# Kernel optimization log

Measured on AMD Instinct MI355X. Metric: run time of the kernel, lower is better.

## Reference

```python
import jax, jax.numpy as jnp
import numpy as np

N = 50000          # nodes
E = 800000         # edges (before self loops)
H = 4              # attention heads
C = 64             # per-head channels
D_IN = 256
NEG_ATT = 0.2      # GATConv attention LeakyReLU slope
NEG_ACT = 0.01     # nn.LeakyReLU default slope
EPS = 1e-5
MLP_DIMS = [64, 32, 16, 2]


def _gat_layer(x, src, dst, W, a_src, a_dst, b, concat):
    """PyG GATConv: gather -> segment-softmax over dst -> scatter-add."""
    n = x.shape[0]
    h = (x @ W).reshape(n, H, C)                       # [N,H,C]
    s = (h * a_src).sum(-1)                            # [N,H]
    d = (h * a_dst).sum(-1)                            # [N,H]
    e = jax.nn.leaky_relu(s[src] + d[dst], NEG_ATT)    # [E',H]
    m = jax.ops.segment_max(e, dst, num_segments=n)    # per-dst max (self loops -> no empty segs)
    w = jnp.exp(e - m[dst])
    den = jax.ops.segment_sum(w, dst, num_segments=n)
    alpha = w / den[dst]                               # [E',H]
    out = jax.ops.segment_sum(alpha[:, :, None] * h[src], dst, num_segments=n)  # [N,H,C]
    out = out.reshape(n, H * C) if concat else out.mean(axis=1)
    return out + b


def _graph_norm(x, w, b, a):
    mu = x.mean(axis=0, keepdims=True)
    y = x - a * mu
    var = (y * y).mean(axis=0, keepdims=True)
    return w * y * jax.lax.rsqrt(var + EPS) + b


def setup_inputs() -> dict:
    key = jax.random.key(0)
    ks = jax.random.split(key, 40)
    d = {
        'x': jax.random.normal(ks[0], (N, D_IN), dtype=jnp.float32),
        'edge_index': jax.random.randint(ks[1], (2, E), 0, N, dtype=jnp.int64),
    }
    dims_in = [D_IN, H * C, H * C]
    norm_dims = [H * C, H * C, C]
    k = 2
    for i in range(3):
        fan = dims_in[i]
        d[f'W{i}'] = jax.random.normal(ks[k], (fan, H * C), dtype=jnp.float32) / np.sqrt(fan); k += 1
        d[f'as{i}'] = jax.random.normal(ks[k], (H, C), dtype=jnp.float32) / np.sqrt(C); k += 1
        d[f'ad{i}'] = jax.random.normal(ks[k], (H, C), dtype=jnp.float32) / np.sqrt(C); k += 1
        d[f'b{i}'] = jnp.zeros((norm_dims[i],), dtype=jnp.float32)
        d[f'gw{i}'] = jnp.ones((norm_dims[i],), dtype=jnp.float32)
        d[f'gb{i}'] = jnp.zeros((norm_dims[i],), dtype=jnp.float32)
        d[f'ga{i}'] = jnp.ones((norm_dims[i],), dtype=jnp.float32)
    for j in range(3):
        fi, fo = MLP_DIMS[j], MLP_DIMS[j + 1]
        d[f'mW{j}'] = jax.random.normal(ks[k], (fi, fo), dtype=jnp.float32) / np.sqrt(fi); k += 1
        d[f'mb{j}'] = jnp.zeros((fo,), dtype=jnp.float32)
    return d


def reference(x, edge_index,
              W0, as0, ad0, b0, gw0, gb0, ga0,
              W1, as1, ad1, b1, gw1, gb1, ga1,
              W2, as2, ad2, b2, gw2, gb2, ga2,
              mW0, mb0, mW1, mb1, mW2, mb2):
    n = x.shape[0]
    loop = jnp.arange(n, dtype=edge_index.dtype)
    src = jnp.concatenate([edge_index[0], loop])   # add self loops (PyG default)
    dst = jnp.concatenate([edge_index[1], loop])

    h = _gat_layer(x, src, dst, W0, as0, ad0, b0, concat=True)
    h = jax.nn.leaky_relu(_graph_norm(h, gw0, gb0, ga0), NEG_ACT)
    h = _gat_layer(h, src, dst, W1, as1, ad1, b1, concat=True)
    h = jax.nn.leaky_relu(_graph_norm(h, gw1, gb1, ga1), NEG_ACT)
    h = _gat_layer(h, src, dst, W2, as2, ad2, b2, concat=False)
    h = jax.nn.leaky_relu(_graph_norm(h, gw2, gb2, ga2), NEG_ACT)

    h = jax.nn.relu(h @ mW0 + mb0)
    h = jax.nn.relu(h @ mW1 + mb1)
    return h @ mW2 + mb2
```

## Files before the change

kernel.cpp:

```cpp
#include <hip/hip_runtime.h>

#define NN 50000
#define EE 800000
#define ET 850000
#define HH 4
#define CC 64
#define FDIM 256

#define SCAN_BLK 512
#define SCAN_NB ((NN + SCAN_BLK - 1) / SCAN_BLK)

typedef unsigned short ushort;
typedef __bf16 bf16x8 __attribute__((ext_vector_type(8)));
typedef float floatx4 __attribute__((ext_vector_type(4)));
typedef ushort ushort8v __attribute__((ext_vector_type(8)));
struct ushort4s { ushort x, y, z, w; };

__device__ __forceinline__ ushort f2bf(float f) {
  union { float f; unsigned u; } v; v.f = f;
  unsigned r = v.u + 0x7fffu + ((v.u >> 16) & 1u);
  return (ushort)(r >> 16);
}
__device__ __forceinline__ float bf2f(ushort u) {
  return __uint_as_float(((unsigned)u) << 16);
}

__device__ __forceinline__ int get_edge(const void* p, int is64, long long idx) {
  if (is64) return (int)((const long long*)p)[idx];
  return ((const int*)p)[idx];
}

__global__ void detect_kernel(const unsigned int* p, int* flag) {
  __shared__ unsigned red[256];
  int t = threadIdx.x;
  unsigned o = 0;
  for (int i = 0; i < 4; i++) o |= p[(t * 4 + i) * 2 + 1];
  red[t] = o;
  __syncthreads();
  for (int s = 128; s > 0; s >>= 1) {
    if (t < s) red[t] |= red[t + s];
    __syncthreads();
  }
  if (t == 0) *flag = (red[0] == 0) ? 1 : 0;
}

__global__ void degree_kernel(const void* eidx, const int* flag, int* deg) {
  int k = blockIdx.x * blockDim.x + threadIdx.x;
  if (k >= ET) return;
  int is64 = *flag;
  int dst = (k < EE) ? get_edge(eidx, is64, (long long)EE + k) : (k - EE);
  atomicAdd(&deg[dst], 1);
}

__global__ __launch_bounds__(SCAN_BLK) void scan1_kernel(const int* __restrict__ deg,
                                                         int* __restrict__ rowptr,
                                                         int* __restrict__ bsum) {
  __shared__ int sm[SCAN_BLK];
  int t = threadIdx.x;
  int i = blockIdx.x * SCAN_BLK + t;
  int v = (i < NN) ? deg[i] : 0;
  sm[t] = v;
  __syncthreads();
#pragma unroll
  for (int o = 1; o < SCAN_BLK; o <<= 1) {
    int u = (t >= o) ? sm[t - o] : 0;
    __syncthreads();
    sm[t] += u;
    __syncthreads();
  }
  if (i < NN) rowptr[i] = sm[t] - v;
  if (t == SCAN_BLK - 1) bsum[blockIdx.x] = sm[t];
}

__global__ __launch_bounds__(128) void scan2_kernel(const int* __restrict__ bsum,
                                                    int* __restrict__ boff,
                                                    int* __restrict__ rowptr) {
  __shared__ int sm[128];
  int t = threadIdx.x;
  int v = (t < SCAN_NB) ? bsum[t] : 0;
  sm[t] = v;
  __syncthreads();
#pragma unroll
  for (int o = 1; o < 128; o <<= 1) {
    int u = (t >= o) ? sm[t - o] : 0;
    __syncthreads();
    sm[t] += u;
    __syncthreads();
  }
  if (t < SCAN_NB) boff[t] = sm[t] - v;
  if (t == 0) rowptr[NN] = ET;
}

__global__ __launch_bounds__(SCAN_BLK) void scan3_kernel(int* __restrict__ rowptr,
                                                         int* __restrict__ cursor,
                                                         const int* __restrict__ boff) {
  int i = blockIdx.x * SCAN_BLK + threadIdx.x;
  if (i >= NN) return;
  int v = rowptr[i] + boff[blockIdx.x];
  rowptr[i] = v;
  cursor[i] = v;
}

__global__ void fill_kernel(const void* eidx, const int* flag, int* cursor, int* csr_src) {
  int k = blockIdx.x * blockDim.x + threadIdx.x;
  if (k >= ET) return;
  int is64 = *flag;
  int src, dst;
  if (k < EE) {
    src = get_edge(eidx, is64, k);
    dst = get_edge(eidx, is64, (long long)EE + k);
  } else {
    src = dst = k - EE;
  }
  int pos = atomicAdd(&cursor[dst], 1);
  csr_src[pos] = src;
}

__global__ void conv_x_kernel(const float* __restrict__ x, ushort* __restrict__ xb) {
  int i = blockIdx.x * 256 + threadIdx.x;
  float4 v = ((const float4*)x)[i];
  ushort4s o;
  o.x = f2bf(v.x); o.y = f2bf(v.y); o.z = f2bf(v.z); o.w = f2bf(v.w);
  ((ushort4s*)xb)[i] = o;
}

__global__ void conv_w_kernel(const float* __restrict__ W, ushort* __restrict__ Wt) {
  int idx = blockIdx.x * 256 + threadIdx.x;
  int k = idx >> 8, n = idx & 255;
  Wt[n * 256 + k] = f2bf(W[idx]);
}

__global__ __launch_bounds__(256) void gemm_bf16(const ushort* __restrict__ A,
                                                 const ushort* __restrict__ Bt,
                                                 ushort* __restrict__ C) {
  __shared__ ushort As[8 * 512];
  __shared__ ushort Bs[8 * 512];
  int tid = threadIdx.x, w = tid >> 6, l = tid & 63;
  int brow0 = blockIdx.x * 128, bcol0 = blockIdx.y * 128;
  int lm = l & 15, lk = (l >> 4) * 8;
  int s0 = 2 * w, s1 = 2 * w + 1;
  int ar0 = min(brow0 + s0 * 16 + lm, NN - 1);
  int ar1 = min(brow0 + s1 * 16 + lm, NN - 1);
  const ushort* ag0 = A + (size_t)ar0 * 256 + lk;
  const ushort* ag1 = A + (size_t)ar1 * 256 + lk;
  const ushort* bg0 = Bt + (size_t)(bcol0 + s0 * 16 + lm) * 256 + lk;
  const ushort* bg1 = Bt + (size_t)(bcol0 + s1 * 16 + lm) * 256 + lk;

  floatx4 acc[4][4];
#pragma unroll
  for (int i = 0; i < 4; i++)
#pragma unroll
    for (int j = 0; j < 4; j++) acc[i][j] = floatx4{0.f, 0.f, 0.f, 0.f};

  int wm = (w >> 1) * 4, wn = (w & 1) * 4;

  for (int k0 = 0; k0 < 256; k0 += 32) {
    ushort8v a0 = *(const ushort8v*)(ag0 + k0);
    ushort8v a1 = *(const ushort8v*)(ag1 + k0);
    ushort8v b0 = *(const ushort8v*)(bg0 + k0);
    ushort8v b1 = *(const ushort8v*)(bg1 + k0);
    *(ushort8v*)&As[s0 * 512 + l * 8] = a0;
    *(ushort8v*)&As[s1 * 512 + l * 8] = a1;
    *(ushort8v*)&Bs[s0 * 512 + l * 8] = b0;
    *(ushort8v*)&Bs[s1 * 512 + l * 8] = b1;
    __syncthreads();
    bf16x8 af[4], bfr[4];
#pragma unroll
    for (int i = 0; i < 4; i++) af[i] = *(const bf16x8*)&As[(wm + i) * 512 + l * 8];
#pragma unroll
    for (int j = 0; j < 4; j++) bfr[j] = *(const bf16x8*)&Bs[(wn + j) * 512 + l * 8];
#pragma unroll
    for (int i = 0; i < 4; i++)
#pragma unroll
      for (int j = 0; j < 4; j++)
        acc[i][j] = __builtin_amdgcn_mfma_f32_16x16x32_bf16(af[i], bfr[j], acc[i][j], 0, 0, 0);
    __syncthreads();
  }

  int quad = l >> 4;
#pragma unroll
  for (int i = 0; i < 4; i++) {
    int r0 = brow0 + (wm + i) * 16 + quad * 4;
#pragma unroll
    for (int j = 0; j < 4; j++) {
      int col = bcol0 + (wn + j) * 16 + lm;
#pragma unroll
      for (int r = 0; r < 4; r++) {
        int row = r0 + r;
        if (row < NN) C[(size_t)row * 256 + col] = f2bf(acc[i][j][r]);
      }
    }
  }
}

__global__ __launch_bounds__(256) void sd_kernel(const ushort* __restrict__ h,
                                                 const float* __restrict__ as_,
                                                 const float* __restrict__ ad_,
                                                 float* __restrict__ s, float* __restrict__ d) {
  int w = threadIdx.x >> 6;
  int l = threadIdx.x & 63;
  int n = blockIdx.x * 4 + w;
  ushort4s hv = *(const ushort4s*)(h + (size_t)n * FDIM + l * 4);
  float4 av = ((const float4*)as_)[l];
  float4 dv = ((const float4*)ad_)[l];
  float f0 = bf2f(hv.x), f1 = bf2f(hv.y), f2 = bf2f(hv.z), f3 = bf2f(hv.w);
  float ps = f0 * av.x + f1 * av.y + f2 * av.z + f3 * av.w;
  float pd = f0 * dv.x + f1 * dv.y + f2 * dv.z + f3 * dv.w;
#pragma unroll
  for (int o = 1; o < 16; o <<= 1) {
    ps += __shfl_xor(ps, o);
    pd += __shfl_xor(pd, o);
  }
  if ((l & 15) == 0) {
    s[n * HH + (l >> 4)] = ps;
    d[n * HH + (l >> 4)] = pd;
  }
}

template <bool CONCAT>
__global__ __launch_bounds__(256) void agg_kernel(const ushort* __restrict__ hb,
                                                  const float* __restrict__ s_arr,
                                                  const float* __restrict__ d_arr,
                                                  const int* __restrict__ rowptr,
                                                  const int* __restrict__ csr_src,
                                                  const float* __restrict__ bias,
                                                  void* __restrict__ outp) {
  int w = __builtin_amdgcn_readfirstlane(threadIdx.x >> 6);
  int l = threadIdx.x & 63;
  int head = l >> 4;
  int n = blockIdx.x * 4 + w;
  int beg = rowptr[n], end = rowptr[n + 1];
  float dh = d_arr[n * HH + head];
  float a0 = 0.f, a1 = 0.f, a2 = 0.f, a3 = 0.f, den = 0.f;

  int i = beg;
  for (; i + 4 <= end; i += 4) {
    int s0 = csr_src[i], s1 = csr_src[i + 1], s2 = csr_src[i + 2], s3 = csr_src[i + 3];
    float e0 = s_arr[s0 * HH + head] + dh;
    float e1 = s_arr[s1 * HH + head] + dh;
    float e2 = s_arr[s2 * HH + head] + dh;
    float e3 = s_arr[s3 * HH + head] + dh;
    ushort4s h0 = *(const ushort4s*)(hb + (unsigned)(s0 * FDIM + l * 4));
    ushort4s h1 = *(const ushort4s*)(hb + (unsigned)(s1 * FDIM + l * 4));
    ushort4s h2 = *(const ushort4s*)(hb + (unsigned)(s2 * FDIM + l * 4));
    ushort4s h3 = *(const ushort4s*)(hb + (unsigned)(s3 * FDIM + l * 4));
    e0 = (e0 > 0.f) ? e0 : 0.2f * e0;  float w0 = __expf(e0);
    e1 = (e1 > 0.f) ? e1 : 0.2f * e1;  float w1 = __expf(e1);
    e2 = (e2 > 0.f) ? e2 : 0.2f * e2;  float w2 = __expf(e2);
    e3 = (e3 > 0.f) ? e3 : 0.2f * e3;  float w3 = __expf(e3);
    den += (w0 + w1) + (w2 + w3);
    a0 = fmaf(w0, bf2f(h0.x), a0); a1 = fmaf(w0, bf2f(h0.y), a1);
    a2 = fmaf(w0, bf2f(h0.z), a2); a3 = fmaf(w0, bf2f(h0.w), a3);
    a0 = fmaf(w1, bf2f(h1.x), a0); a1 = fmaf(w1, bf2f(h1.y), a1);
    a2 = fmaf(w1, bf2f(h1.z), a2); a3 = fmaf(w1, bf2f(h1.w), a3);
    a0 = fmaf(w2, bf2f(h2.x), a0); a1 = fmaf(w2, bf2f(h2.y), a1);
    a2 = fmaf(w2, bf2f(h2.z), a2); a3 = fmaf(w2, bf2f(h2.w), a3);
    a0 = fmaf(w3, bf2f(h3.x), a0); a1 = fmaf(w3, bf2f(h3.y), a1);
    a2 = fmaf(w3, bf2f(h3.z), a2); a3 = fmaf(w3, bf2f(h3.w), a3);
  }
  for (; i < end; i++) {
    int s0 = csr_src[i];
    float e0 = s_arr[s0 * HH + head] + dh;
    ushort4s h0 = *(const ushort4s*)(hb + (unsigned)(s0 * FDIM + l * 4));
    e0 = (e0 > 0.f) ? e0 : 0.2f * e0;
    float w0 = __expf(e0);
    den += w0;
    a0 = fmaf(w0, bf2f(h0.x), a0); a1 = fmaf(w0, bf2f(h0.y), a1);
    a2 = fmaf(w0, bf2f(h0.z), a2); a3 = fmaf(w0, bf2f(h0.w), a3);
  }
  float inv = 1.0f / den;
  float r0 = a0 * inv, r1 = a1 * inv, r2 = a2 * inv, r3 = a3 * inv;

  if (CONCAT) {
    float4 bv = ((const float4*)bias)[l];
    ushort4s o;
    o.x = f2bf(r0 + bv.x); o.y = f2bf(r1 + bv.y);
    o.z = f2bf(r2 + bv.z); o.w = f2bf(r3 + bv.w);
    ((ushort4s*)outp)[(unsigned)(n * 64 + l)] = o;
  } else {
    r0 += __shfl_xor(r0, 16); r1 += __shfl_xor(r1, 16);
    r2 += __shfl_xor(r2, 16); r3 += __shfl_xor(r3, 16);
    r0 += __shfl_xor(r0, 32); r1 += __shfl_xor(r1, 32);
    r2 += __shfl_xor(r2, 32); r3 += __shfl_xor(r3, 32);
    if (l < 16) {
      float4 bv = ((const float4*)bias)[l];
      float4 o;
      o.x = 0.25f * r0 + bv.x; o.y = 0.25f * r1 + bv.y;
      o.z = 0.25f * r2 + bv.z; o.w = 0.25f * r3 + bv.w;
      ((float4*)outp)[(unsigned)(n * 16 + l)] = o;
    }
  }
}

__global__ __launch_bounds__(256) void norm_reduce_bf(const ushort* __restrict__ xin,
                                                      float* colsum, float* colsumsq) {
  int f = threadIdx.x;
  int r0 = blockIdx.x * 128;
  int r1 = min(NN, r0 + 128);
  float s1 = 0.f, s2 = 0.f;
  for (int r = r0; r < r1; r++) {
    float v = bf2f(xin[(size_t)r * FDIM + f]);
    s1 += v; s2 += v * v;
  }
  atomicAdd(&colsum[f], s1);
  atomicAdd(&colsumsq[f], s2);
}

__global__ __launch_bounds__(256) void norm_reduce_f32(const float* __restrict__ xin,
                                                       float* colsum, float* colsumsq) {
  int f = threadIdx.x & (CC - 1);
  int rl = threadIdx.x / CC;
  int r0 = blockIdx.x * 128;
  int r1 = min(NN, r0 + 128);
  float s1 = 0.f, s2 = 0.f;
  for (int r = r0 + rl; r < r1; r += 4) {
    float v = xin[(size_t)r * CC + f];
    s1 += v; s2 += v * v;
  }
  atomicAdd(&colsum[f], s1);
  atomicAdd(&colsumsq[f], s2);
}

__global__ __launch_bounds__(256) void norm_apply_bf(const ushort* __restrict__ in,
                                                     ushort* __restrict__ outb,
                                                     const float* __restrict__ colsum,
                                                     const float* __restrict__ colsumsq,
                                                     const float* __restrict__ ga,
                                                     const float* __restrict__ gw,
                                                     const float* __restrict__ gb) {
  __shared__ float sc[FDIM], sh[FDIM];
  int t = threadIdx.x;
  {
    const float invn = 1.0f / (float)NN;
    float mu = colsum[t] * invn;
    float ex2 = colsumsq[t] * invn;
    float a = ga[t];
    float var = fmaxf(ex2 - (2.f * a - a * a) * mu * mu, 0.f);
    float s = gw[t] * rsqrtf(var + 1e-5f);
    sc[t] = s; sh[t] = gb[t] - s * a * mu;
  }
  __syncthreads();
  const int total = NN * FDIM / 4;
  for (int i = blockIdx.x * 256 + t; i < total; i += gridDim.x * 256) {
    int f0 = (i * 4) & (FDIM - 1);
    ushort4s v = ((const ushort4s*)in)[i];
    float y0 = sc[f0 + 0] * bf2f(v.x) + sh[f0 + 0];
    float y1 = sc[f0 + 1] * bf2f(v.y) + sh[f0 + 1];
    float y2 = sc[f0 + 2] * bf2f(v.z) + sh[f0 + 2];
    float y3 = sc[f0 + 3] * bf2f(v.w) + sh[f0 + 3];
    ushort4s o;
    o.x = f2bf((y0 > 0.f) ? y0 : 0.01f * y0);
    o.y = f2bf((y1 > 0.f) ? y1 : 0.01f * y1);
    o.z = f2bf((y2 > 0.f) ? y2 : 0.01f * y2);
    o.w = f2bf((y3 > 0.f) ? y3 : 0.01f * y3);
    ((ushort4s*)outb)[i] = o;
  }
}

__global__ __launch_bounds__(256) void norm_apply_f32(float* __restrict__ xio,
                                                      const float* __restrict__ colsum,
                                                      const float* __restrict__ colsumsq,
                                                      const float* __restrict__ ga,
                                                      const float* __restrict__ gw,
                                                      const float* __restrict__ gb) {
  __shared__ float sc[CC], sh[CC];
  int t = threadIdx.x;
  if (t < CC) {
    const float invn = 1.0f / (float)NN;
    float mu = colsum[t] * invn;
    float ex2 = colsumsq[t] * invn;
    float a = ga[t];
    float var = fmaxf(ex2 - (2.f * a - a * a) * mu * mu, 0.f);
    float s = gw[t] * rsqrtf(var + 1e-5f);
    sc[t] = s; sh[t] = gb[t] - s * a * mu;
  }
  __syncthreads();
  const int total = NN * CC;
  for (int i = blockIdx.x * 256 + t; i < total; i += gridDim.x * 256) {
    int f = i & (CC - 1);
    float y = sc[f] * xio[i] + sh[f];
    xio[i] = (y > 0.f) ? y : 0.01f * y;
  }
}

__global__ __launch_bounds__(256) void mlp_kernel(const float* __restrict__ xin,
                                                  const float* mW0, const float* mb0,
                                                  const float* mW1, const float* mb1,
                                                  const float* mW2, const float* mb2,
                                                  float* __restrict__ out) {
  __shared__ float W0s[64 * 32];
  __shared__ float W1s[32 * 16];
  __shared__ float W2s[16 * 2];
  __shared__ float b0s[32], b1s[16], b2s[2];
  int t = threadIdx.x;
  for (int i = t; i < 2048; i += 256) W0s[i] = mW0[i];
  for (int i = t; i < 512; i += 256) W1s[i] = mW1[i];
  if (t < 32) { W2s[t] = mW2[t]; b0s[t] = mb0[t]; }
  if (t < 16) b1s[t] = mb1[t];
  if (t < 2) b2s[t] = mb2[t];
  __syncthreads();
  int node = blockIdx.x * 256 + t;
  if (node >= NN) return;
  float in[64];
  const float* xr = xin + (size_t)node * 64;
#pragma unroll
  for (int k = 0; k < 64; k++) in[k] = xr[k];
  float h1[32];
#pragma unroll
  for (int j = 0; j < 32; j++) h1[j] = b0s[j];
#pragma unroll
  for (int k = 0; k < 64; k++) {
    float v = in[k];
#pragma unroll
    for (int j = 0; j < 32; j++) h1[j] += v * W0s[k * 32 + j];
  }
#pragma unroll
  for (int j = 0; j < 32; j++) h1[j] = fmaxf(h1[j], 0.f);
  float h2[16];
#pragma unroll
  for (int j = 0; j < 16; j++) h2[j] = b1s[j];
#pragma unroll
  for (int k = 0; k < 32; k++) {
    float v = h1[k];
#pragma unroll
    for (int j = 0; j < 16; j++) h2[j] += v * W1s[k * 16 + j];
  }
#pragma unroll
  for (int j = 0; j < 16; j++) h2[j] = fmaxf(h2[j], 0.f);
  float o0 = b2s[0], o1 = b2s[1];
#pragma unroll
  for (int k = 0; k < 16; k++) {
    o0 += h2[k] * W2s[k * 2 + 0];
    o1 += h2[k] * W2s[k * 2 + 1];
  }
  out[(size_t)node * 2 + 0] = o0;
  out[(size_t)node * 2 + 1] = o1;
}

extern "C" void kernel_launch(void* const* d_in, const int* in_sizes, int n_in,
                              void* d_out, int out_size, void* d_ws, size_t ws_size,
                              hipStream_t stream) {
  const float* x = (const float*)d_in[0];
  const void* ei = d_in[1];
  const float* W[3]   = {(const float*)d_in[2],  (const float*)d_in[9],  (const float*)d_in[16]};
  const float* as_[3] = {(const float*)d_in[3],  (const float*)d_in[10], (const float*)d_in[17]};
  const float* ad_[3] = {(const float*)d_in[4],  (const float*)d_in[11], (const float*)d_in[18]};
  const float* b_[3]  = {(const float*)d_in[5],  (const float*)d_in[12], (const float*)d_in[19]};
  const float* gw[3]  = {(const float*)d_in[6],  (const float*)d_in[13], (const float*)d_in[20]};
  const float* gb[3]  = {(const float*)d_in[7],  (const float*)d_in[14], (const float*)d_in[21]};
  const float* ga[3]  = {(const float*)d_in[8],  (const float*)d_in[15], (const float*)d_in[22]};
  const float* mW0 = (const float*)d_in[23];
  const float* mb0 = (const float*)d_in[24];
  const float* mW1 = (const float*)d_in[25];
  const float* mb1 = (const float*)d_in[26];
  const float* mW2 = (const float*)d_in[27];
  const float* mb2 = (const float*)d_in[28];
  float* out = (float*)d_out;

  char* ws = (char*)d_ws;
  size_t off = 0;
  auto take = [&](size_t bytes) -> char* {
    char* p = ws + off;
    off = (off + bytes + 255) & ~(size_t)255;
    return p;
  };
  ushort* xb    = (ushort*)take((size_t)NN * FDIM * 2);
  ushort* hb    = (ushort*)take((size_t)NN * FDIM * 2);
  ushort* yb    = (ushort*)take((size_t)NN * FDIM * 2);
  ushort* aggb  = (ushort*)take((size_t)NN * FDIM * 2);
  float* bufD   = (float*)take((size_t)NN * CC * 4);
  ushort* Wt[3];
  for (int i = 0; i < 3; i++) Wt[i] = (ushort*)take((size_t)256 * 256 * 2);
  float* s_arr  = (float*)take((size_t)NN * HH * 4);
  float* d_arr  = (float*)take((size_t)NN * HH * 4);
  int* deg      = (int*)take((size_t)NN * 4);
  int* cursor   = (int*)take((size_t)NN * 4);
  int* rowptr   = (int*)take((size_t)(NN + 1) * 4);
  int* csr_src  = (int*)take((size_t)ET * 4);
  int* bsum     = (int*)take(512);
  int* boff     = (int*)take(512);
  float* colsum   = (float*)take(1024);
  float* colsumsq = (float*)take(1024);
  int* flag       = (int*)take(256);

  hipMemsetAsync(deg, 0, (size_t)NN * 4, stream);
  detect_kernel<<<1, 256, 0, stream>>>((const unsigned int*)ei, flag);
  degree_kernel<<<(ET + 255) / 256, 256, 0, stream>>>(ei, flag, deg);
  scan1_kernel<<<SCAN_NB, SCAN_BLK, 0, stream>>>(deg, rowptr, bsum);
  scan2_kernel<<<1, 128, 0, stream>>>(bsum, boff, rowptr);
  scan3_kernel<<<SCAN_NB, SCAN_BLK, 0, stream>>>(rowptr, cursor, boff);
  fill_kernel<<<(ET + 255) / 256, 256, 0, stream>>>(ei, flag, cursor, csr_src);

  conv_x_kernel<<<(NN * FDIM / 4 + 255) / 256, 256, 0, stream>>>(x, xb);
  for (int L = 0; L < 3; L++)
    conv_w_kernel<<<256, 256, 0, stream>>>(W[L], Wt[L]);

  const ushort* lin = xb;
  for (int L = 0; L < 3; L++) {
    gemm_bf16<<<dim3((NN + 127) / 128, 2), 256, 0, stream>>>(lin, Wt[L], hb);
    sd_kernel<<<NN / 4, 256, 0, stream>>>(hb, as_[L], ad_[L], s_arr, d_arr);
    hipMemsetAsync(colsum, 0, 2048, stream);
    if (L < 2) {
      agg_kernel<true><<<NN / 4, 256, 0, stream>>>(hb, s_arr, d_arr, rowptr, csr_src, b_[L], aggb);
      norm_reduce_bf<<<(NN + 127) / 128, 256, 0, stream>>>(aggb, colsum, colsumsq);
      norm_apply_bf<<<1024, 256, 0, stream>>>(aggb, yb, colsum, colsumsq, ga[L], gw[L], gb[L]);
      lin = yb;
    } else {
      agg_kernel<false><<<NN / 4, 256, 0, stream>>>(hb, s_arr, d_arr, rowptr, csr_src, b_[L], bufD);
      norm_reduce_f32<<<(NN + 127) / 128, 256, 0, stream>>>(bufD, colsum, colsumsq);
      norm_apply_f32<<<512, 256, 0, stream>>>(bufD, colsum, colsumsq, ga[L], gw[L], gb[L]);
    }
  }
  mlp_kernel<<<(NN + 255) / 256, 256, 0, stream>>>(bufD, mW0, mb0, mW1, mb1, mW2, mb2, out);
}
```

Baseline: 714.3 us.

## Fuse final norm into MLP, use direct-to-LDS GEMM loads, vectorize norm reduce

Folds the last GraphNorm apply and LeakyReLU into the MLP kernel, which removes one full read-write pass over the 50000x64 buffer and one launch. The GEMM now fills shared memory with global_load_lds instead of staging each tile through registers. The bf16 column reduction switches to 4-wide loads across four row groups, combined through LDS before the atomics. The three weight conversions now run as a single launch. The global_load_lds path depends on the lane-to-LDS layout of the builtin matching the previous manual store layout.

```diff
diff --git a/kernel.cpp b/kernel.cpp
--- a/kernel.cpp
+++ b/kernel.cpp
@@ -15,6 +15,9 @@
 typedef float floatx4 __attribute__((ext_vector_type(4)));
 typedef ushort ushort8v __attribute__((ext_vector_type(8)));
 struct ushort4s { ushort x, y, z, w; };
+
+#define GLOBAL_AS __attribute__((address_space(1)))
+#define LDS_AS __attribute__((address_space(3)))
 
 __device__ __forceinline__ ushort f2bf(float f) {
   union { float f; unsigned u; } v; v.f = f;
@@ -124,7 +127,12 @@
   ((ushort4s*)xb)[i] = o;
 }
 
-__global__ void conv_w_kernel(const float* __restrict__ W, ushort* __restrict__ Wt) {
+__global__ void conv_w_kernel(const float* __restrict__ W0, const float* __restrict__ W1,
+                              const float* __restrict__ W2,
+                              ushort* __restrict__ T0, ushort* __restrict__ T1,
+                              ushort* __restrict__ T2) {
+  const float* W = (blockIdx.y == 0) ? W0 : (blockIdx.y == 1) ? W1 : W2;
+  ushort* Wt = (blockIdx.y == 0) ? T0 : (blockIdx.y == 1) ? T1 : T2;
   int idx = blockIdx.x * 256 + threadIdx.x;
   int k = idx >> 8, n = idx & 255;
   Wt[n * 256 + k] = f2bf(W[idx]);
@@ -155,14 +163,14 @@
   int wm = (w >> 1) * 4, wn = (w & 1) * 4;
 
   for (int k0 = 0; k0 < 256; k0 += 32) {
-    ushort8v a0 = *(const ushort8v*)(ag0 + k0);
-    ushort8v a1 = *(const ushort8v*)(ag1 + k0);
-    ushort8v b0 = *(const ushort8v*)(bg0 + k0);
-    ushort8v b1 = *(const ushort8v*)(bg1 + k0);
-    *(ushort8v*)&As[s0 * 512 + l * 8] = a0;
-    *(ushort8v*)&As[s1 * 512 + l * 8] = a1;
-    *(ushort8v*)&Bs[s0 * 512 + l * 8] = b0;
-    *(ushort8v*)&Bs[s1 * 512 + l * 8] = b1;
+    __builtin_amdgcn_global_load_lds((const GLOBAL_AS void*)(ag0 + k0),
+                                     (LDS_AS void*)&As[s0 * 512], 16, 0, 0);
+    __builtin_amdgcn_global_load_lds((const GLOBAL_AS void*)(ag1 + k0),
+                                     (LDS_AS void*)&As[s1 * 512], 16, 0, 0);
+    __builtin_amdgcn_global_load_lds((const GLOBAL_AS void*)(bg0 + k0),
+                                     (LDS_AS void*)&Bs[s0 * 512], 16, 0, 0);
+    __builtin_amdgcn_global_load_lds((const GLOBAL_AS void*)(bg1 + k0),
+                                     (LDS_AS void*)&Bs[s1 * 512], 16, 0, 0);
     __syncthreads();
     bf16x8 af[4], bfr[4];
 #pragma unroll
@@ -294,16 +302,37 @@
 
 __global__ __launch_bounds__(256) void norm_reduce_bf(const ushort* __restrict__ xin,
                                                       float* colsum, float* colsumsq) {
-  int f = threadIdx.x;
+  __shared__ float4 sm1[256], sm2[256];
+  int t = threadIdx.x;
+  int c4 = (t & 63) * 4;
+  int rl = t >> 6;
   int r0 = blockIdx.x * 128;
   int r1 = min(NN, r0 + 128);
-  float s1 = 0.f, s2 = 0.f;
-  for (int r = r0; r < r1; r++) {
-    float v = bf2f(xin[(size_t)r * FDIM + f]);
-    s1 += v; s2 += v * v;
-  }
-  atomicAdd(&colsum[f], s1);
-  atomicAdd(&colsumsq[f], s2);
+  float s0 = 0.f, s1 = 0.f, s2 = 0.f, s3 = 0.f;
+  float q0 = 0.f, q1 = 0.f, q2 = 0.f, q3 = 0.f;
+  for (int r = r0 + rl; r < r1; r += 4) {
+    ushort4s v = *(const ushort4s*)(xin + (size_t)r * FDIM + c4);
+    float f0 = bf2f(v.x), f1 = bf2f(v.y), f2 = bf2f(v.z), f3 = bf2f(v.w);
+    s0 += f0; q0 += f0 * f0;
+    s1 += f1; q1 += f1 * f1;
+    s2 += f2; q2 += f2 * f2;
+    s3 += f3; q3 += f3 * f3;
+  }
+  sm1[t] = float4{s0, s1, s2, s3};
+  sm2[t] = float4{q0, q1, q2, q3};
+  __syncthreads();
+  if (t < 64) {
+    float4 a = sm1[t], b = sm1[t + 64], c = sm1[t + 128], d = sm1[t + 192];
+    atomicAdd(&colsum[c4 + 0], a.x + b.x + c.x + d.x);
+    atomicAdd(&colsum[c4 + 1], a.y + b.y + c.y + d.y);
+    atomicAdd(&colsum[c4 + 2], a.z + b.z + c.z + d.z);
+    atomicAdd(&colsum[c4 + 3], a.w + b.w + c.w + d.w);
+    float4 e = sm2[t], f = sm2[t + 64], g = sm2[t + 128], h = sm2[t + 192];
+    atomicAdd(&colsumsq[c4 + 0], e.x + f.x + g.x + h.x);
+    atomicAdd(&colsumsq[c4 + 1], e.y + f.y + g.y + h.y);
+    atomicAdd(&colsumsq[c4 + 2], e.z + f.z + g.z + h.z);
+    atomicAdd(&colsumsq[c4 + 3], e.w + f.w + g.w + h.w);
+  }
 }
 
 __global__ __launch_bounds__(256) void norm_reduce_f32(const float* __restrict__ xin,
@@ -357,14 +386,27 @@
   }
 }
 
-__global__ __launch_bounds__(256) void norm_apply_f32(float* __restrict__ xio,
-                                                      const float* __restrict__ colsum,
-                                                      const float* __restrict__ colsumsq,
-                                                      const float* __restrict__ ga,
-                                                      const float* __restrict__ gw,
-                                                      const float* __restrict__ gb) {
+__global__ __launch_bounds__(256) void mlp_kernel(const float* __restrict__ xin,
+                                                  const float* __restrict__ colsum,
+                                                  const float* __restrict__ colsumsq,
+                                                  const float* __restrict__ ga,
+                                                  const float* __restrict__ gw,
+                                                  const float* __restrict__ gb,
+                                                  const float* mW0, const float* mb0,
+                                                  const float* mW1, const float* mb1,
+                                                  const float* mW2, const float* mb2,
+                                                  float* __restrict__ out) {
+  __shared__ float W0s[64 * 32];
+  __shared__ float W1s[32 * 16];
+  __shared__ float W2s[16 * 2];
+  __shared__ float b0s[32], b1s[16], b2s[2];
   __shared__ float sc[CC], sh[CC];
   int t = threadIdx.x;
+  for (int i = t; i < 2048; i += 256) W0s[i] = mW0[i];
+  for (int i = t; i < 512; i += 256) W1s[i] = mW1[i];
+  if (t < 32) { W2s[t] = mW2[t]; b0s[t] = mb0[t]; }
+  if (t < 16) b1s[t] = mb1[t];
+  if (t < 2) b2s[t] = mb2[t];
   if (t < CC) {
     const float invn = 1.0f / (float)NN;
     float mu = colsum[t] * invn;
@@ -375,36 +417,15 @@
     sc[t] = s; sh[t] = gb[t] - s * a * mu;
   }
   __syncthreads();
-  const int total = NN * CC;
-  for (int i = blockIdx.x * 256 + t; i < total; i += gridDim.x * 256) {
-    int f = i & (CC - 1);
-    float y = sc[f] * xio[i] + sh[f];
-    xio[i] = (y > 0.f) ? y : 0.01f * y;
-  }
-}
-
-__global__ __launch_bounds__(256) void mlp_kernel(const float* __restrict__ xin,
-                                                  const float* mW0, const float* mb0,
-                                                  const float* mW1, const float* mb1,
-                                                  const float* mW2, const float* mb2,
-                                                  float* __restrict__ out) {
-  __shared__ float W0s[64 * 32];
-  __shared__ float W1s[32 * 16];
-  __shared__ float W2s[16 * 2];
-  __shared__ float b0s[32], b1s[16], b2s[2];
-  int t = threadIdx.x;
-  for (int i = t; i < 2048; i += 256) W0s[i] = mW0[i];
-  for (int i = t; i < 512; i += 256) W1s[i] = mW1[i];
-  if (t < 32) { W2s[t] = mW2[t]; b0s[t] = mb0[t]; }
-  if (t < 16) b1s[t] = mb1[t];
-  if (t < 2) b2s[t] = mb2[t];
-  __syncthreads();
   int node = blockIdx.x * 256 + t;
   if (node >= NN) return;
   float in[64];
   const float* xr = xin + (size_t)node * 64;
 #pragma unroll
-  for (int k = 0; k < 64; k++) in[k] = xr[k];
+  for (int k = 0; k < 64; k++) {
+    float y = sc[k] * xr[k] + sh[k];
+    in[k] = (y > 0.f) ? y : 0.01f * y;
+  }
   float h1[32];
 #pragma unroll
   for (int j = 0; j < 32; j++) h1[j] = b0s[j];
@@ -473,15 +494,15 @@
   for (int i = 0; i < 3; i++) Wt[i] = (ushort*)take((size_t)256 * 256 * 2);
   float* s_arr  = (float*)take((size_t)NN * HH * 4);
   float* d_arr  = (float*)take((size_t)NN * HH * 4);
+  float* colsum   = (float*)take(1024);
+  float* colsumsq = (float*)take(1024);
   int* deg      = (int*)take((size_t)NN * 4);
   int* cursor   = (int*)take((size_t)NN * 4);
   int* rowptr   = (int*)take((size_t)(NN + 1) * 4);
   int* csr_src  = (int*)take((size_t)ET * 4);
   int* bsum     = (int*)take(512);
   int* boff     = (int*)take(512);
-  float* colsum   = (float*)take(1024);
-  float* colsumsq = (float*)take(1024);
-  int* flag       = (int*)take(256);
+  int* flag     = (int*)take(256);
 
   hipMemsetAsync(deg, 0, (size_t)NN * 4, stream);
   detect_kernel<<<1, 256, 0, stream>>>((const unsigned int*)ei, flag);
@@ -492,8 +513,7 @@
   fill_kernel<<<(ET + 255) / 256, 256, 0, stream>>>(ei, flag, cursor, csr_src);
 
   conv_x_kernel<<<(NN * FDIM / 4 + 255) / 256, 256, 0, stream>>>(x, xb);
-  for (int L = 0; L < 3; L++)
-    conv_w_kernel<<<256, 256, 0, stream>>>(W[L], Wt[L]);
+  conv_w_kernel<<<dim3(256, 3), 256, 0, stream>>>(W[0], W[1], W[2], Wt[0], Wt[1], Wt[2]);
 
   const ushort* lin = xb;
   for (int L = 0; L < 3; L++) {
@@ -508,8 +528,9 @@
     } else {
       agg_kernel<false><<<NN / 4, 256, 0, stream>>>(hb, s_arr, d_arr, rowptr, csr_src, b_[L], bufD);
       norm_reduce_f32<<<(NN + 127) / 128, 256, 0, stream>>>(bufD, colsum, colsumsq);
-      norm_apply_f32<<<512, 256, 0, stream>>>(bufD, colsum, colsumsq, ga[L], gw[L], gb[L]);
     }
   }
-  mlp_kernel<<<(NN + 255) / 256, 256, 0, stream>>>(bufD, mW0, mb0, mW1, mb1, mW2, mb2, out);
-}
+  mlp_kernel<<<(NN + 255) / 256, 256, 0, stream>>>(bufD, colsum, colsumsq,
+                                                   ga[2], gw[2], gb[2],
+                                                   mW0, mb0, mW1, mb1, mW2, mb2, out);
+}
```

New measurement: 726.6 us. About the same (+1.7%).
